# Performance work log

Measured on AMD Instinct MI355X. Metric: run time of the kernel, lower is better.

The kernel has to match this reference:

```python
import jax, jax.numpy as jnp
import numpy as np

B, Q, K = 4, 128, 1024
DQ, DK, DV, H = 512, 512, 512, 256
NEG_INF = -1e6


def setup_inputs() -> dict:
    key = jax.random.key(0)
    ks = jax.random.split(key, 6)
    queries = jax.random.normal(ks[0], (B, Q, DQ), dtype=jnp.float32)
    keys = jax.random.normal(ks[1], (B, K, DK), dtype=jnp.float32)
    values = jax.random.normal(ks[2], (B, K, DV), dtype=jnp.float32)
    valid_lens = jax.random.randint(ks[3], (B,), 1, K + 1, dtype=jnp.int32)
    # Learned params (Dense use_bias=False): W_q [DQ,H], W_k [DK,H], w_v [H] (Dense(1) squeezed)
    Wq = jax.random.normal(ks[4], (DQ, H), dtype=jnp.float32) / np.sqrt(DQ)
    Wk = jax.random.normal(ks[5], (DK, H), dtype=jnp.float32) / np.sqrt(DK)
    wv = jax.random.normal(jax.random.fold_in(key, 7), (H,), dtype=jnp.float32) / np.sqrt(H)
    return {"queries": queries, "keys": keys, "values": values,
            "valid_lens": valid_lens, "Wq": Wq, "Wk": Wk, "wv": wv}


def reference(queries, keys, values, valid_lens, Wq, Wk, wv):
    q = queries @ Wq                       # [B,Q,H]
    k = keys @ Wk                          # [B,K,H]
    feats = jnp.tanh(q[:, :, None, :] + k[:, None, :, :])   # [B,Q,K,H]
    scores = jnp.einsum('bqkh,h->bqk', feats, wv)            # [B,Q,K]
    mask = jnp.arange(scores.shape[-1]) < valid_lens[:, None, None]  # [B,1,K]
    scores = jnp.where(mask, scores, NEG_INF)
    attn = jax.nn.softmax(scores, axis=-1)                   # [B,Q,K]
    # dropout is identity at inference
    return attn @ values                                     # [B,Q,DV]
```

## Files before the change

kernel.cpp:

```cpp
#include <hip/hip_runtime.h>

#define Bn 4
#define Qn 128
#define Kn 1024
#define Dn 512
#define Hn 256

__device__ __forceinline__ float fast_tanh(float x) {
    float e = __expf(2.0f * x);
    return 1.0f - 2.0f * __builtin_amdgcn_rcpf(1.0f + e);
}

#define PBK 64

__global__ __launch_bounds__(256) void proj_kernel(
    const float* __restrict__ queries, const float* __restrict__ keys,
    const float* __restrict__ Wq, const float* __restrict__ Wk,
    const int* __restrict__ valid_lens,
    float* __restrict__ qproj, float* __restrict__ kproj)
{
    const int blk = blockIdx.x;
    const int nt = blk & 3;
    const int mt = blk >> 2;
    const int t = threadIdx.x;
    const float* Asrc; const float* W; float* Dst;
    int m0;
    if (mt < 8) {
        m0 = mt * 64;
        Asrc = queries; W = Wq; Dst = qproj;
    } else {
        int r0 = (mt - 8) * 64;
        int b = r0 >> 10;
        if ((r0 & 1023) >= valid_lens[b]) return;
        m0 = r0;
        Asrc = keys; W = Wk; Dst = kproj;
    }
    const int n0 = nt * 64;

    __shared__ float s_a[PBK][68];
    __shared__ float s_b[PBK][64];

    const int trow = t >> 4;
    const int tcol = t & 15;

    float acc[4][4] = {{0.f}};
    float4 ra[4], rb[4];

    #pragma unroll
    for (int i = 0; i < 4; ++i) {
        int row = (t >> 4) + i * 16, c4 = t & 15;
        ra[i] = *(const float4*)(Asrc + (size_t)(m0 + row) * Dn + c4 * 4);
        rb[i] = *(const float4*)(W + (size_t)row * Hn + n0 + c4 * 4);
    }

    for (int kt = 0; kt < 8; ++kt) {
        __syncthreads();
        #pragma unroll
        for (int i = 0; i < 4; ++i) {
            int row = (t >> 4) + i * 16, c4 = t & 15;
            s_a[c4 * 4 + 0][row] = ra[i].x;
            s_a[c4 * 4 + 1][row] = ra[i].y;
            s_a[c4 * 4 + 2][row] = ra[i].z;
            s_a[c4 * 4 + 3][row] = ra[i].w;
            *(float4*)&s_b[row][c4 * 4] = rb[i];
        }
        __syncthreads();
        if (kt < 7) {
            const int d0n = (kt + 1) * PBK;
            #pragma unroll
            for (int i = 0; i < 4; ++i) {
                int row = (t >> 4) + i * 16, c4 = t & 15;
                ra[i] = *(const float4*)(Asrc + (size_t)(m0 + row) * Dn + d0n + c4 * 4);
                rb[i] = *(const float4*)(W + (size_t)(d0n + row) * Hn + n0 + c4 * 4);
            }
        }
        #pragma unroll 16
        for (int kk = 0; kk < PBK; ++kk) {
            float4 a4 = *(const float4*)&s_a[kk][trow * 4];
            float4 b4 = *(const float4*)&s_b[kk][tcol * 4];
            float a[4] = {a4.x, a4.y, a4.z, a4.w};
            float b[4] = {b4.x, b4.y, b4.z, b4.w};
            #pragma unroll
            for (int i = 0; i < 4; ++i)
                #pragma unroll
                for (int j = 0; j < 4; ++j)
                    acc[i][j] += a[i] * b[j];
        }
    }
    #pragma unroll
    for (int i = 0; i < 4; ++i) {
        float4 o; o.x = acc[i][0]; o.y = acc[i][1]; o.z = acc[i][2]; o.w = acc[i][3];
        *(float4*)(Dst + (size_t)(m0 + trow * 4 + i) * Hn + n0 + tcol * 4) = o;
    }
}

#define SK_KT 16
#define SK_PAD 260

__global__ __launch_bounds__(256) void score_kernel(
    const float* __restrict__ qproj, const float* __restrict__ kproj,
    const float* __restrict__ wv, const int* __restrict__ valid_lens,
    float* __restrict__ escores, float* __restrict__ rowsum)
{
    const int blk = blockIdx.x;
    const int kt = blk & 63;
    const int qt = (blk >> 6) & 31;
    const int b  = blk >> 11;
    const int vlen = valid_lens[b];
    const int k0 = kt * SK_KT;
    if (k0 >= vlen) return;
    const int q0 = qt * 4;
    const int t = threadIdx.x;

    __shared__ float s_k[SK_KT * SK_PAD];
    __shared__ float s_q[4 * Hn];
    __shared__ float s_wv[Hn];

    {
        const float4* src = reinterpret_cast<const float4*>(
            kproj + ((size_t)b * Kn + k0) * Hn);
        #pragma unroll
        for (int i = 0; i < 4; ++i) {
            int idx = t + i * 256;
            int row = idx >> 6, c4 = idx & 63;
            *reinterpret_cast<float4*>(&s_k[row * SK_PAD + c4 * 4]) = src[idx];
        }
        reinterpret_cast<float4*>(s_q)[t] = reinterpret_cast<const float4*>(
            qproj + ((size_t)b * Qn + q0) * Hn)[t];
        if (t < 64)
            reinterpret_cast<float4*>(s_wv)[t] =
                reinterpret_cast<const float4*>(wv)[t];
    }
    __syncthreads();

    const int wave = t >> 6;
    const int lane = t & 63;
    const int kloc = lane & 15;
    const int hq   = lane >> 4;

    const float4* kr = reinterpret_cast<const float4*>(&s_k[kloc * SK_PAD + hq * 64]);
    const float4* qr = reinterpret_cast<const float4*>(&s_q[wave * Hn + hq * 64]);
    const float4* wr = reinterpret_cast<const float4*>(&s_wv[hq * 64]);

    float s = 0.0f;
    #pragma unroll
    for (int i = 0; i < 16; ++i) {
        float4 kv = kr[i];
        float4 qv = qr[i];
        float4 wq = wr[i];
        s += wq.x * fast_tanh(qv.x + kv.x);
        s += wq.y * fast_tanh(qv.y + kv.y);
        s += wq.z * fast_tanh(qv.z + kv.z);
        s += wq.w * fast_tanh(qv.w + kv.w);
    }
    s += __shfl_xor(s, 16, 64);
    s += __shfl_xor(s, 32, 64);

    const int k = k0 + kloc;
    float e = 0.0f;
    if (lane < 16 && k < vlen) {
        e = __expf(s);
        escores[((size_t)b * Qn + q0 + wave) * Kn + k] = e;
    }
    #pragma unroll
    for (int off = 32; off; off >>= 1)
        e += __shfl_xor(e, off, 64);
    if (lane == 0)
        atomicAdd(&rowsum[b * Qn + q0 + wave], e);
}

__global__ __launch_bounds__(256) void av_part_kernel(
    const float* __restrict__ escores, const float* __restrict__ values,
    float* __restrict__ parts)
{
    const int blk = blockIdx.x;
    const int kc = blk & 3;
    const int dh = (blk >> 2) & 1;
    const int qt = (blk >> 3) & 15;
    const int b  = blk >> 7;
    const int t = threadIdx.x;
    const int q0 = qt * 8;
    const int kb = kc * 256;
    const int d  = dh * 256 + t;

    __shared__ float s_e[8][256];
    #pragma unroll
    for (int i = 0; i < 2; ++i) {
        int idx = t + i * 256;
        int row = idx >> 6, c4 = idx & 63;
        *(float4*)&s_e[row][c4 * 4] = *(const float4*)(
            escores + ((size_t)(b * Qn + q0 + row)) * Kn + kb + c4 * 4);
    }
    __syncthreads();

    const float* vb = values + ((size_t)b * Kn + kb) * Dn + d;
    float acc[8] = {0.f};
    #pragma unroll 2
    for (int k = 0; k < 256; k += 4) {
        float v0 = vb[(size_t)(k + 0) * Dn];
        float v1 = vb[(size_t)(k + 1) * Dn];
        float v2 = vb[(size_t)(k + 2) * Dn];
        float v3 = vb[(size_t)(k + 3) * Dn];
        #pragma unroll
        for (int j = 0; j < 8; ++j) {
            float4 e4 = *(const float4*)&s_e[j][k];
            acc[j] += e4.x * v0 + e4.y * v1 + e4.z * v2 + e4.w * v3;
        }
    }
    float* pp = parts + (size_t)kc * (Bn * Qn * Dn)
                      + ((size_t)(b * Qn + q0)) * Dn + d;
    #pragma unroll
    for (int j = 0; j < 8; ++j)
        pp[(size_t)j * Dn] = acc[j];
}

__global__ __launch_bounds__(256) void reduce_kernel(
    const float* __restrict__ parts, const float* __restrict__ rowsum,
    float* __restrict__ out)
{
    const int idx = blockIdx.x * 256 + threadIdx.x;
    const int row = (idx * 4) >> 9;
    const float inv = __builtin_amdgcn_rcpf(rowsum[row]);
    const float4* p = (const float4*)parts;
    float4 a = p[idx];
    float4 b = p[idx + 65536];
    float4 c = p[idx + 131072];
    float4 d = p[idx + 196608];
    float4 o;
    o.x = (a.x + b.x + c.x + d.x) * inv;
    o.y = (a.y + b.y + c.y + d.y) * inv;
    o.z = (a.z + b.z + c.z + d.z) * inv;
    o.w = (a.w + b.w + c.w + d.w) * inv;
    ((float4*)out)[idx] = o;
}

extern "C" void kernel_launch(void* const* d_in, const int* in_sizes, int n_in,
                              void* d_out, int out_size, void* d_ws, size_t ws_size,
                              hipStream_t stream) {
    const float* queries    = (const float*)d_in[0];
    const float* keys       = (const float*)d_in[1];
    const float* values     = (const float*)d_in[2];
    const int*   valid_lens = (const int*)  d_in[3];
    const float* Wq         = (const float*)d_in[4];
    const float* Wk         = (const float*)d_in[5];
    const float* wv         = (const float*)d_in[6];
    float* out = (float*)d_out;

    float* qproj   = (float*)d_ws;
    float* kproj   = qproj + Bn * Qn * Hn;
    float* escores = kproj + Bn * Kn * Hn;
    float* rowsum  = escores + Bn * Qn * Kn;
    float* parts   = kproj;

    hipMemsetAsync(escores, 0, (size_t)(Bn * Qn * Kn + Bn * Qn) * sizeof(float),
                   stream);
    proj_kernel<<<288, 256, 0, stream>>>(queries, keys, Wq, Wk, valid_lens,
                                         qproj, kproj);
    score_kernel<<<Bn * 32 * 64, 256, 0, stream>>>(qproj, kproj, wv,
                                                   valid_lens, escores, rowsum);
    av_part_kernel<<<512, 256, 0, stream>>>(escores, values, parts);
    reduce_kernel<<<256, 256, 0, stream>>>(parts, rowsum, out);
}
```

Baseline: 171.2 us.

## Restructure projection split-K, register-blocked score kernel with exp2 tanh algebra

Pre-scales the projections by 2*log2(e) so tanh becomes 1 - 2/(1+exp2(q+k)), and computes each score as sum(wv) minus twice a weighted sum of reciprocals, which removes multiplies per element. The score kernel is rebuilt to give each lane one key and four queries, with keys transposed in shared memory and queries and wv read through the scalar/cache path. The key projection is split along the reduction into two partial buffers that the score kernel adds together, and the projection GEMM reads W straight from global memory. The AV kernel now reads escores from global memory instead of staging them in LDS. The trade-offs are more workspace, an extra pass over the partial key buffers, and heavier reliance on the caches.

```diff
diff --git a/kernel.cpp b/kernel.cpp
--- a/kernel.cpp
+++ b/kernel.cpp
@@ -5,171 +5,226 @@
 #define Kn 1024
 #define Dn 512
 #define Hn 256
-
-__device__ __forceinline__ float fast_tanh(float x) {
-    float e = __expf(2.0f * x);
-    return 1.0f - 2.0f * __builtin_amdgcn_rcpf(1.0f + e);
-}
-
-#define PBK 64
-
-__global__ __launch_bounds__(256) void proj_kernel(
+#define SCALE 2.8853900817779268f
+#define LOG2E 1.4426950408889634f
+
+__global__ __launch_bounds__(128) void proj_kernel(
     const float* __restrict__ queries, const float* __restrict__ keys,
     const float* __restrict__ Wq, const float* __restrict__ Wk,
     const int* __restrict__ valid_lens,
-    float* __restrict__ qproj, float* __restrict__ kproj)
+    float* __restrict__ qproj, float* __restrict__ kpart0,
+    float* __restrict__ kpart1)
 {
     const int blk = blockIdx.x;
-    const int nt = blk & 3;
-    const int mt = blk >> 2;
     const int t = threadIdx.x;
-    const float* Asrc; const float* W; float* Dst;
-    int m0;
-    if (mt < 8) {
-        m0 = mt * 64;
-        Asrc = queries; W = Wq; Dst = qproj;
-    } else {
-        int r0 = (mt - 8) * 64;
-        int b = r0 >> 10;
-        if ((r0 & 1023) >= valid_lens[b]) return;
-        m0 = r0;
-        Asrc = keys; W = Wk; Dst = kproj;
-    }
-    const int n0 = nt * 64;
-
-    __shared__ float s_a[PBK][68];
-    __shared__ float s_b[PBK][64];
-
-    const int trow = t >> 4;
-    const int tcol = t & 15;
-
-    float acc[4][4] = {{0.f}};
-    float4 ra[4], rb[4];
-
-    #pragma unroll
-    for (int i = 0; i < 4; ++i) {
-        int row = (t >> 4) + i * 16, c4 = t & 15;
-        ra[i] = *(const float4*)(Asrc + (size_t)(m0 + row) * Dn + c4 * 4);
-        rb[i] = *(const float4*)(W + (size_t)row * Hn + n0 + c4 * 4);
-    }
-
-    for (int kt = 0; kt < 8; ++kt) {
-        __syncthreads();
+    __shared__ float s_a[64][68];
+
+    if (blk < 64) {
+        const int nt = blk & 3, mtq = blk >> 2;
+        const int m0 = mtq * 32, n0 = nt * 64;
+        const int trow = t >> 3, tcol = t & 7;
+        const float* Wb = Wq + n0 + tcol * 8;
+        float acc[2][8];
+        #pragma unroll
+        for (int i = 0; i < 2; ++i)
+            #pragma unroll
+            for (int j = 0; j < 8; ++j) acc[i][j] = 0.f;
+
+        float4 ra[4];
         #pragma unroll
         for (int i = 0; i < 4; ++i) {
-            int row = (t >> 4) + i * 16, c4 = t & 15;
-            s_a[c4 * 4 + 0][row] = ra[i].x;
-            s_a[c4 * 4 + 1][row] = ra[i].y;
-            s_a[c4 * 4 + 2][row] = ra[i].z;
-            s_a[c4 * 4 + 3][row] = ra[i].w;
-            *(float4*)&s_b[row][c4 * 4] = rb[i];
-        }
-        __syncthreads();
-        if (kt < 7) {
-            const int d0n = (kt + 1) * PBK;
+            int idx = t + i * 128, r = idx >> 4, cc = idx & 15;
+            ra[i] = *(const float4*)(queries + (size_t)(m0 + r) * Dn + cc * 4);
+        }
+        for (int kt = 0; kt < 8; ++kt) {
+            __syncthreads();
             #pragma unroll
             for (int i = 0; i < 4; ++i) {
-                int row = (t >> 4) + i * 16, c4 = t & 15;
-                ra[i] = *(const float4*)(Asrc + (size_t)(m0 + row) * Dn + d0n + c4 * 4);
-                rb[i] = *(const float4*)(W + (size_t)(d0n + row) * Hn + n0 + c4 * 4);
-            }
-        }
-        #pragma unroll 16
-        for (int kk = 0; kk < PBK; ++kk) {
-            float4 a4 = *(const float4*)&s_a[kk][trow * 4];
-            float4 b4 = *(const float4*)&s_b[kk][tcol * 4];
-            float a[4] = {a4.x, a4.y, a4.z, a4.w};
-            float b[4] = {b4.x, b4.y, b4.z, b4.w};
+                int idx = t + i * 128, r = idx >> 4, cc = idx & 15;
+                s_a[cc +  0][r] = ra[i].x;
+                s_a[cc + 16][r] = ra[i].y;
+                s_a[cc + 32][r] = ra[i].z;
+                s_a[cc + 48][r] = ra[i].w;
+            }
+            __syncthreads();
+            if (kt < 7) {
+                const int d0n = (kt + 1) * 64;
+                #pragma unroll
+                for (int i = 0; i < 4; ++i) {
+                    int idx = t + i * 128, r = idx >> 4, cc = idx & 15;
+                    ra[i] = *(const float4*)(queries + (size_t)(m0 + r) * Dn + d0n + cc * 4);
+                }
+            }
+            #pragma unroll 16
+            for (int r = 0; r < 64; ++r) {
+                const int ko = 4 * (r & 15) + (r >> 4);
+                float2 a2 = *(const float2*)&s_a[r][trow * 2];
+                const float* wb = Wb + (size_t)(kt * 64 + ko) * Hn;
+                float4 b0 = *(const float4*)wb;
+                float4 b1 = *(const float4*)(wb + 4);
+                float bb[8] = {b0.x,b0.y,b0.z,b0.w,b1.x,b1.y,b1.z,b1.w};
+                #pragma unroll
+                for (int j = 0; j < 8; ++j) {
+                    acc[0][j] += a2.x * bb[j];
+                    acc[1][j] += a2.y * bb[j];
+                }
+            }
+        }
+        #pragma unroll
+        for (int i = 0; i < 2; ++i) {
+            float* dst = qproj + (size_t)(m0 + trow * 2 + i) * Hn + n0 + tcol * 8;
+            float4 o0, o1;
+            o0.x = acc[i][0]*SCALE; o0.y = acc[i][1]*SCALE;
+            o0.z = acc[i][2]*SCALE; o0.w = acc[i][3]*SCALE;
+            o1.x = acc[i][4]*SCALE; o1.y = acc[i][5]*SCALE;
+            o1.z = acc[i][6]*SCALE; o1.w = acc[i][7]*SCALE;
+            *(float4*)dst = o0; *(float4*)(dst + 4) = o1;
+        }
+    } else {
+        const int bk = blk - 64;
+        const int kc = bk & 1, nt = (bk >> 1) & 3, mt = bk >> 3;
+        const int m0 = mt * 64;
+        if ((m0 & 1023) >= valid_lens[m0 >> 10]) return;
+        const int n0 = nt * 64;
+        const int trow = t >> 3, tcol = t & 7;
+        const int dbase = kc * 256;
+        const float* Wb = Wk + (size_t)dbase * Hn + n0 + tcol * 8;
+        float* kpart = kc ? kpart1 : kpart0;
+        float acc[4][8];
+        #pragma unroll
+        for (int i = 0; i < 4; ++i)
             #pragma unroll
-            for (int i = 0; i < 4; ++i)
+            for (int j = 0; j < 8; ++j) acc[i][j] = 0.f;
+
+        float4 ra[8];
+        #pragma unroll
+        for (int i = 0; i < 8; ++i) {
+            int idx = t + i * 128, r = idx >> 4, cc = idx & 15;
+            ra[i] = *(const float4*)(keys + (size_t)(m0 + r) * Dn + dbase + cc * 4);
+        }
+        for (int kt = 0; kt < 4; ++kt) {
+            __syncthreads();
+            #pragma unroll
+            for (int i = 0; i < 8; ++i) {
+                int idx = t + i * 128, r = idx >> 4, cc = idx & 15;
+                s_a[cc +  0][r] = ra[i].x;
+                s_a[cc + 16][r] = ra[i].y;
+                s_a[cc + 32][r] = ra[i].z;
+                s_a[cc + 48][r] = ra[i].w;
+            }
+            __syncthreads();
+            if (kt < 3) {
+                const int d0n = dbase + (kt + 1) * 64;
                 #pragma unroll
-                for (int j = 0; j < 4; ++j)
-                    acc[i][j] += a[i] * b[j];
+                for (int i = 0; i < 8; ++i) {
+                    int idx = t + i * 128, r = idx >> 4, cc = idx & 15;
+                    ra[i] = *(const float4*)(keys + (size_t)(m0 + r) * Dn + d0n + cc * 4);
+                }
+            }
+            #pragma unroll 16
+            for (int r = 0; r < 64; ++r) {
+                const int ko = 4 * (r & 15) + (r >> 4);
+                float4 a4 = *(const float4*)&s_a[r][trow * 4];
+                const float* wb = Wb + (size_t)(kt * 64 + ko) * Hn;
+                float4 b0 = *(const float4*)wb;
+                float4 b1 = *(const float4*)(wb + 4);
+                float aa[4] = {a4.x, a4.y, a4.z, a4.w};
+                float bb[8] = {b0.x,b0.y,b0.z,b0.w,b1.x,b1.y,b1.z,b1.w};
+                #pragma unroll
+                for (int i = 0; i < 4; ++i)
+                    #pragma unroll
+                    for (int j = 0; j < 8; ++j)
+                        acc[i][j] += aa[i] * bb[j];
+            }
+        }
+        #pragma unroll
+        for (int i = 0; i < 4; ++i) {
+            float* dst = kpart + (size_t)(m0 + trow * 4 + i) * Hn + n0 + tcol * 8;
+            float4 o0, o1;
+            o0.x = acc[i][0]*SCALE; o0.y = acc[i][1]*SCALE;
+            o0.z = acc[i][2]*SCALE; o0.w = acc[i][3]*SCALE;
+            o1.x = acc[i][4]*SCALE; o1.y = acc[i][5]*SCALE;
+            o1.z = acc[i][6]*SCALE; o1.w = acc[i][7]*SCALE;
+            *(float4*)dst = o0; *(float4*)(dst + 4) = o1;
         }
     }
-    #pragma unroll
-    for (int i = 0; i < 4; ++i) {
-        float4 o; o.x = acc[i][0]; o.y = acc[i][1]; o.z = acc[i][2]; o.w = acc[i][3];
-        *(float4*)(Dst + (size_t)(m0 + trow * 4 + i) * Hn + n0 + tcol * 4) = o;
-    }
-}
-
-#define SK_KT 16
-#define SK_PAD 260
+}
 
 __global__ __launch_bounds__(256) void score_kernel(
-    const float* __restrict__ qproj, const float* __restrict__ kproj,
-    const float* __restrict__ wv, const int* __restrict__ valid_lens,
+    const float* __restrict__ qproj, const float* __restrict__ kpart0,
+    const float* __restrict__ kpart1, const float* __restrict__ wv,
+    const int* __restrict__ valid_lens,
     float* __restrict__ escores, float* __restrict__ rowsum)
 {
     const int blk = blockIdx.x;
-    const int kt = blk & 63;
-    const int qt = (blk >> 6) & 31;
-    const int b  = blk >> 11;
+    const int kt = blk & 15;
+    const int qt = (blk >> 4) & 7;
+    const int b  = blk >> 7;
     const int vlen = valid_lens[b];
-    const int k0 = kt * SK_KT;
+    const int k0 = kt * 64;
     if (k0 >= vlen) return;
-    const int q0 = qt * 4;
     const int t = threadIdx.x;
-
-    __shared__ float s_k[SK_KT * SK_PAD];
-    __shared__ float s_q[4 * Hn];
-    __shared__ float s_wv[Hn];
-
-    {
-        const float4* src = reinterpret_cast<const float4*>(
-            kproj + ((size_t)b * Kn + k0) * Hn);
-        #pragma unroll
-        for (int i = 0; i < 4; ++i) {
+    const int wave = __builtin_amdgcn_readfirstlane(t >> 6);
+    const int lane = t & 63;
+
+    __shared__ float s_kT[128][64];
+
+    const float* qb = qproj + (size_t)(b * Qn + qt * 16 + wave * 4) * Hn;
+    float acc2[4] = {0.f, 0.f, 0.f, 0.f};
+    float sumw = 0.f;
+
+    for (int ph = 0; ph < 2; ++ph) {
+        __syncthreads();
+        #pragma unroll
+        for (int i = 0; i < 8; ++i) {
             int idx = t + i * 256;
-            int row = idx >> 6, c4 = idx & 63;
-            *reinterpret_cast<float4*>(&s_k[row * SK_PAD + c4 * 4]) = src[idx];
-        }
-        reinterpret_cast<float4*>(s_q)[t] = reinterpret_cast<const float4*>(
-            qproj + ((size_t)b * Qn + q0) * Hn)[t];
-        if (t < 64)
-            reinterpret_cast<float4*>(s_wv)[t] =
-                reinterpret_cast<const float4*>(wv)[t];
+            int k = idx & 63, h4 = idx >> 6;
+            size_t off = (size_t)(b * Kn + k0 + k) * Hn + ph * 128 + h4 * 4;
+            float4 p0 = *(const float4*)(kpart0 + off);
+            float4 p1 = *(const float4*)(kpart1 + off);
+            s_kT[h4 * 4 + 0][k] = p0.x + p1.x;
+            s_kT[h4 * 4 + 1][k] = p0.y + p1.y;
+            s_kT[h4 * 4 + 2][k] = p0.z + p1.z;
+            s_kT[h4 * 4 + 3][k] = p0.w + p1.w;
+        }
+        __syncthreads();
+        #pragma unroll 4
+        for (int h = 0; h < 128; ++h) {
+            const int hg = ph * 128 + h;
+            const float kv = s_kT[h][lane];
+            const float wvh = wv[hg];
+            const float q0 = qb[0 * Hn + hg];
+            const float q1 = qb[1 * Hn + hg];
+            const float q2 = qb[2 * Hn + hg];
+            const float q3 = qb[3 * Hn + hg];
+            sumw += wvh;
+            float r0 = __builtin_amdgcn_rcpf(1.f + exp2f(q0 + kv));
+            float r1 = __builtin_amdgcn_rcpf(1.f + exp2f(q1 + kv));
+            float r2 = __builtin_amdgcn_rcpf(1.f + exp2f(q2 + kv));
+            float r3 = __builtin_amdgcn_rcpf(1.f + exp2f(q3 + kv));
+            acc2[0] = fmaf(wvh, r0, acc2[0]);
+            acc2[1] = fmaf(wvh, r1, acc2[1]);
+            acc2[2] = fmaf(wvh, r2, acc2[2]);
+            acc2[3] = fmaf(wvh, r3, acc2[3]);
+        }
     }
-    __syncthreads();
-
-    const int wave = t >> 6;
-    const int lane = t & 63;
-    const int kloc = lane & 15;
-    const int hq   = lane >> 4;
-
-    const float4* kr = reinterpret_cast<const float4*>(&s_k[kloc * SK_PAD + hq * 64]);
-    const float4* qr = reinterpret_cast<const float4*>(&s_q[wave * Hn + hq * 64]);
-    const float4* wr = reinterpret_cast<const float4*>(&s_wv[hq * 64]);
-
-    float s = 0.0f;
+
+    const int k = k0 + lane;
     #pragma unroll
-    for (int i = 0; i < 16; ++i) {
-        float4 kv = kr[i];
-        float4 qv = qr[i];
-        float4 wq = wr[i];
-        s += wq.x * fast_tanh(qv.x + kv.x);
-        s += wq.y * fast_tanh(qv.y + kv.y);
-        s += wq.z * fast_tanh(qv.z + kv.z);
-        s += wq.w * fast_tanh(qv.w + kv.w);
+    for (int j = 0; j < 4; ++j) {
+        float s = sumw - 2.f * acc2[j];
+        float e = (k < vlen) ? exp2f(s * LOG2E) : 0.f;
+        if (k < vlen)
+            escores[(size_t)(b * Qn + qt * 16 + wave * 4 + j) * Kn + k] = e;
+        #pragma unroll
+        for (int off = 32; off; off >>= 1)
+            e += __shfl_xor(e, off, 64);
+        if (lane == 0)
+            atomicAdd(&rowsum[b * Qn + qt * 16 + wave * 4 + j], e);
     }
-    s += __shfl_xor(s, 16, 64);
-    s += __shfl_xor(s, 32, 64);
-
-    const int k = k0 + kloc;
-    float e = 0.0f;
-    if (lane < 16 && k < vlen) {
-        e = __expf(s);
-        escores[((size_t)b * Qn + q0 + wave) * Kn + k] = e;
-    }
-    #pragma unroll
-    for (int off = 32; off; off >>= 1)
-        e += __shfl_xor(e, off, 64);
-    if (lane == 0)
-        atomicAdd(&rowsum[b * Qn + q0 + wave], e);
-}
-
-__global__ __launch_bounds__(256) void av_part_kernel(
+}
+
+__global__ __launch_bounds__(256) void av_kernel(
     const float* __restrict__ escores, const float* __restrict__ values,
     float* __restrict__ parts)
 {
@@ -179,22 +234,12 @@
     const int qt = (blk >> 3) & 15;
     const int b  = blk >> 7;
     const int t = threadIdx.x;
-    const int q0 = qt * 8;
-    const int kb = kc * 256;
-    const int d  = dh * 256 + t;
-
-    __shared__ float s_e[8][256];
-    #pragma unroll
-    for (int i = 0; i < 2; ++i) {
-        int idx = t + i * 256;
-        int row = idx >> 6, c4 = idx & 63;
-        *(float4*)&s_e[row][c4 * 4] = *(const float4*)(
-            escores + ((size_t)(b * Qn + q0 + row)) * Kn + kb + c4 * 4);
-    }
-    __syncthreads();
-
+    const int q0 = qt * 8, kb = kc * 256, d = dh * 256 + t;
+
+    const int ebase = __builtin_amdgcn_readfirstlane((b * Qn + q0) * Kn + kb);
     const float* vb = values + ((size_t)b * Kn + kb) * Dn + d;
-    float acc[8] = {0.f};
+
+    float acc[8] = {0.f, 0.f, 0.f, 0.f, 0.f, 0.f, 0.f, 0.f};
     #pragma unroll 2
     for (int k = 0; k < 256; k += 4) {
         float v0 = vb[(size_t)(k + 0) * Dn];
@@ -203,12 +248,11 @@
         float v3 = vb[(size_t)(k + 3) * Dn];
         #pragma unroll
         for (int j = 0; j < 8; ++j) {
-            float4 e4 = *(const float4*)&s_e[j][k];
+            float4 e4 = *(const float4*)(escores + ebase + j * Kn + k);
             acc[j] += e4.x * v0 + e4.y * v1 + e4.z * v2 + e4.w * v3;
         }
     }
-    float* pp = parts + (size_t)kc * (Bn * Qn * Dn)
-                      + ((size_t)(b * Qn + q0)) * Dn + d;
+    float* pp = parts + (size_t)kc * (Bn * Qn * Dn) + (size_t)(b * Qn + q0) * Dn + d;
     #pragma unroll
     for (int j = 0; j < 8; ++j)
         pp[(size_t)j * Dn] = acc[j];
@@ -247,17 +291,18 @@
     float* out = (float*)d_out;
 
     float* qproj   = (float*)d_ws;
-    float* kproj   = qproj + Bn * Qn * Hn;
-    float* escores = kproj + Bn * Kn * Hn;
+    float* kpart0  = qproj + Bn * Qn * Hn;
+    float* kpart1  = kpart0 + Bn * Kn * Hn;
+    float* escores = kpart1 + Bn * Kn * Hn;
     float* rowsum  = escores + Bn * Qn * Kn;
-    float* parts   = kproj;
+    float* parts   = rowsum + Bn * Qn;
 
     hipMemsetAsync(escores, 0, (size_t)(Bn * Qn * Kn + Bn * Qn) * sizeof(float),
                    stream);
-    proj_kernel<<<288, 256, 0, stream>>>(queries, keys, Wq, Wk, valid_lens,
-                                         qproj, kproj);
-    score_kernel<<<Bn * 32 * 64, 256, 0, stream>>>(qproj, kproj, wv,
-                                                   valid_lens, escores, rowsum);
-    av_part_kernel<<<512, 256, 0, stream>>>(escores, values, parts);
+    proj_kernel<<<576, 128, 0, stream>>>(queries, keys, Wq, Wk, valid_lens,
+                                         qproj, kpart0, kpart1);
+    score_kernel<<<512, 256, 0, stream>>>(qproj, kpart0, kpart1, wv,
+                                          valid_lens, escores, rowsum);
+    av_kernel<<<512, 256, 0, stream>>>(escores, values, parts);
     reduce_kernel<<<256, 256, 0, stream>>>(parts, rowsum, out);
 }
```

Result: slower. 273.0 us (+59.5%).
